# Kernel tuning notes

Measured on AMD Instinct MI355X. Metric: run time of the kernel, lower is better.

The kernel has to match this reference:

```python
import jax, jax.numpy as jnp
import numpy as np
import math

B, S, D, H = 8, 2048, 1024, 16
DH = D // H  # attention head size = 64

def setup_inputs() -> dict:
    key = jax.random.key(0)
    ks = jax.random.split(key, 10)
    s = 1.0 / math.sqrt(D)
    return {
        "hidden_states": jax.random.normal(ks[0], (B, S, D), dtype=jnp.float32),
        "attention_mask": jnp.zeros((B, 1, S), dtype=jnp.float32),
        "Wq": jax.random.normal(ks[1], (D, D), dtype=jnp.float32) * s,
        "bq": jnp.zeros((D,), dtype=jnp.float32),
        "Wqa": jax.random.normal(ks[2], (D, H), dtype=jnp.float32) * s,
        "bqa": jnp.zeros((H,), dtype=jnp.float32),
        "Wk": jax.random.normal(ks[3], (D, D), dtype=jnp.float32) * s,
        "bk": jnp.zeros((D,), dtype=jnp.float32),
        "Wt": jax.random.normal(ks[4], (D, D), dtype=jnp.float32) * s,
        "bt": jnp.zeros((D,), dtype=jnp.float32),
    }

def reference(hidden_states, attention_mask, Wq, bq, Wqa, bqa, Wk, bk, Wt, bt):
    scale = 1.0 / math.sqrt(DH)
    q = hidden_states @ Wq + bq                      # [B,S,D] mixed_query_layer
    k = hidden_states @ Wk + bk                      # [B,S,D] mixed_key_layer
    # query attention logits -> [B,H,S]
    q_score = jnp.swapaxes(q @ Wqa + bqa, 1, 2) * scale + attention_mask
    q_weight = jax.nn.softmax(q_score, axis=-1)      # [B,H,S]
    ql = jnp.swapaxes(q.reshape(B, S, H, DH), 1, 2)  # [B,H,S,DH]
    kl = jnp.swapaxes(k.reshape(B, S, H, DH), 1, 2)  # [B,H,S,DH]
    pooled_q = jnp.einsum('bhs,bhsd->bhd', q_weight, ql)          # [B,H,DH]
    qk_score = jnp.einsum('bhsd,bhd->bhs', kl, pooled_q) * scale + attention_mask
    qk_weight = jax.nn.softmax(qk_score, axis=-1)                 # [B,H,S]
    pooled_k = jnp.einsum('bhs,bhsd->bhd', qk_weight, kl)         # [B,H,DH]
    weighted = pooled_k[:, :, None, :] * ql                       # [B,H,S,DH]
    weighted = jnp.swapaxes(weighted, 1, 2).reshape(B, S, D)      # [B,S,D]
    out = weighted @ Wt + bt + q                                  # transform + residual to query
    return out
```

## Files before the change

### kernel.cpp

```cpp
#include <hip/hip_runtime.h>
#include <hip/hip_bf16.h>
#include <math.h>

#define BB 8
#define SS 2048
#define DD 1024
#define HH 16
#define DHH 64
#define NROWS (BB*SS)
#define QSLICE ((size_t)BB * HH * SS)

typedef unsigned short u16;
typedef __attribute__((ext_vector_type(8))) __bf16 bf16x8;
typedef __attribute__((ext_vector_type(4))) float f32x4;

__device__ __forceinline__ u16 f2bf(float f) {
    union { float f; unsigned u; } v; v.f = f;
    unsigned r = v.u + 0x7fffu + ((v.u >> 16) & 1u);
    return (u16)(r >> 16);
}
__device__ __forceinline__ float bf2f(u16 b) {
    union { unsigned u; float f; } v; v.u = ((unsigned)b) << 16;
    return v.f;
}

__device__ __forceinline__ void load_lds16(const void* g, void* l) {
    __builtin_amdgcn_global_load_lds(
        (const __attribute__((address_space(1))) unsigned int*)g,
        (__attribute__((address_space(3))) unsigned int*)l,
        16, 0, 0);
}

__global__ __launch_bounds__(256) void cast_bf16_kernel(const float* __restrict__ in,
                                                        u16* __restrict__ out, int n4) {
    int i = blockIdx.x * 256 + threadIdx.x;
    if (i >= n4) return;
    float4 v = ((const float4*)in)[i];
    ushort4 o;
    o.x = f2bf(v.x); o.y = f2bf(v.y); o.z = f2bf(v.z); o.w = f2bf(v.w);
    ((ushort4*)out)[i] = o;
}

__global__ __launch_bounds__(256) void transpose_cast_kernel(const float* __restrict__ W,
                                                             u16* __restrict__ WT) {
    __shared__ float tile[32][33];
    int m0 = blockIdx.x * 32, k0 = blockIdx.y * 32;
    int tx = threadIdx.x & 31, ty = threadIdx.x >> 5;
    #pragma unroll
    for (int i = 0; i < 4; i++) {
        int kk = ty + i * 8;
        tile[kk][tx] = W[(k0 + kk) * DD + m0 + tx];
    }
    __syncthreads();
    #pragma unroll
    for (int i = 0; i < 4; i++) {
        int mm = ty + i * 8;
        WT[(m0 + mm) * DD + k0 + tx] = f2bf(tile[tx][mm]);
    }
}

__global__ __launch_bounds__(256) void wqa_transpose_kernel(const float* __restrict__ Wqa,
                                                            u16* __restrict__ WqaT) {
    int i = blockIdx.x * 256 + threadIdx.x;
    int h = i >> 10, k = i & 1023;
    WqaT[i] = f2bf(Wqa[k * HH + h]);
}

template<int MODE>
__global__ __launch_bounds__(256)
void gemm_kernel(const u16* __restrict__ A, const u16* __restrict__ BT,
                 const float* __restrict__ bias, const u16* __restrict__ res,
                 float* __restrict__ Cf, u16* __restrict__ Cb) {
    __shared__ u16 sA[128 * 64];
    __shared__ u16 sB[128 * 64];
    const int row0 = blockIdx.x * 128;
    const int col0 = blockIdx.y * 128;
    const int t = threadIdx.x;
    const int w = t >> 6, lane = t & 63;
    const int wr = (w >> 1) * 64, wc = (w & 1) * 64;
    const int m16 = lane & 15, quad = lane >> 4;

    f32x4 acc[4][4];
    #pragma unroll
    for (int i = 0; i < 4; i++)
        #pragma unroll
        for (int j = 0; j < 4; j++)
            acc[i][j] = (f32x4){0.f, 0.f, 0.f, 0.f};

    const int srow = t >> 3;
    const int scol = ((t & 7) ^ (srow & 7)) * 8;
    const u16* Ag = A + (size_t)(row0 + srow) * DD + scol;
    const u16* Bg = BT + (size_t)(col0 + srow) * DD + scol;

    for (int k0 = 0; k0 < DD; k0 += 64) {
        __syncthreads();
        #pragma unroll
        for (int j = 0; j < 4; j++) {
            load_lds16(Ag + k0 + (size_t)j * 32 * DD, &sA[j * 2048 + t * 8]);
            load_lds16(Bg + k0 + (size_t)j * 32 * DD, &sB[j * 2048 + t * 8]);
        }
        __syncthreads();
        #pragma unroll
        for (int ks = 0; ks < 2; ks++) {
            const int cpos = ((ks * 4 + quad) ^ (m16 & 7)) * 8;
            bf16x8 af[4], bfr[4];
            #pragma unroll
            for (int i = 0; i < 4; i++) {
                af[i]  = *(const bf16x8*)&sA[(wr + i * 16 + m16) * 64 + cpos];
                bfr[i] = *(const bf16x8*)&sB[(wc + i * 16 + m16) * 64 + cpos];
            }
            #pragma unroll
            for (int mi = 0; mi < 4; mi++)
                #pragma unroll
                for (int ni = 0; ni < 4; ni++)
                    acc[mi][ni] = __builtin_amdgcn_mfma_f32_16x16x32_bf16(
                        af[mi], bfr[ni], acc[mi][ni], 0, 0, 0);
        }
    }

    #pragma unroll
    for (int mi = 0; mi < 4; mi++) {
        #pragma unroll
        for (int r = 0; r < 4; r++) {
            int row = row0 + wr + mi * 16 + quad * 4 + r;
            #pragma unroll
            for (int ni = 0; ni < 4; ni++) {
                int col = col0 + wc + ni * 16 + m16;
                float v = acc[mi][ni][r] + bias[col];
                size_t idx = (size_t)row * DD + col;
                if (MODE == 1) Cb[idx] = f2bf(v);
                else Cf[idx] = v + bf2f(res[idx]);
            }
        }
    }
}

__global__ __launch_bounds__(256)
void qscore_mfma_kernel(const u16* __restrict__ qbf, const u16* __restrict__ WqaT,
                        float* __restrict__ qraw) {
    int w = threadIdx.x >> 6, lane = threadIdx.x & 63;
    int row0 = blockIdx.x * 64 + w * 16;
    int kbase = blockIdx.y * 256;
    int m16 = lane & 15, quad = lane >> 4;
    f32x4 acc = (f32x4){0.f, 0.f, 0.f, 0.f};
    const u16* ap = qbf + (size_t)(row0 + m16) * DD + kbase + quad * 8;
    const u16* bp = WqaT + (size_t)m16 * DD + kbase + quad * 8;
    #pragma unroll
    for (int kk = 0; kk < 256; kk += 32) {
        bf16x8 a = *(const bf16x8*)(ap + kk);
        bf16x8 b = *(const bf16x8*)(bp + kk);
        acc = __builtin_amdgcn_mfma_f32_16x16x32_bf16(a, b, acc, 0, 0, 0);
    }
    #pragma unroll
    for (int r = 0; r < 4; r++) {
        int grow = row0 + quad * 4 + r;
        int b = grow >> 11, sidx = grow & 2047;
        qraw[((size_t)(blockIdx.y * BB + b) * HH + m16) * SS + sidx] = acc[r];
    }
}

template<bool EPI>
__global__ __launch_bounds__(256)
void softmax_kernel(float* __restrict__ score, const float* __restrict__ bqa,
                    const float* __restrict__ mask) {
    int bh = blockIdx.x;
    int b = bh >> 4, h = bh & 15;
    float* srow = score + ((size_t)bh << 11);
    __shared__ float rm[4], rs[4];
    int t = threadIdx.x;

    float v[8];
    float m = -1e30f;
    #pragma unroll
    for (int i = 0; i < 8; i++) {
        int off = t + i * 256;
        float x;
        if (EPI) {
            x = srow[off] + srow[off + QSLICE] + srow[off + 2 * QSLICE] + srow[off + 3 * QSLICE];
            x = (x + bqa[h]) * 0.125f + mask[b * SS + off];
        } else {
            x = srow[off];
        }
        v[i] = x; m = fmaxf(m, x);
    }
    #pragma unroll
    for (int off = 32; off; off >>= 1) m = fmaxf(m, __shfl_xor(m, off));
    if ((t & 63) == 0) rm[t >> 6] = m;
    __syncthreads();
    m = fmaxf(fmaxf(rm[0], rm[1]), fmaxf(rm[2], rm[3]));

    float sum = 0.f;
    #pragma unroll
    for (int i = 0; i < 8; i++) { v[i] = __expf(v[i] - m); sum += v[i]; }
    #pragma unroll
    for (int off = 32; off; off >>= 1) sum += __shfl_xor(sum, off);
    if ((t & 63) == 0) rs[t >> 6] = sum;
    __syncthreads();
    float inv = 1.0f / (rs[0] + rs[1] + rs[2] + rs[3]);
    #pragma unroll
    for (int i = 0; i < 8; i++) srow[t + i * 256] = v[i] * inv;
}

__global__ __launch_bounds__(256)
void pool_kernel(const float* __restrict__ w, const u16* __restrict__ X,
                 float* __restrict__ pooled) {
    int b = blockIdx.x;
    int s0 = blockIdx.y * 32;
    int t = threadIdx.x;
    int wid = t >> 6, lane = t & 63;
    int h = lane >> 2;
    __shared__ float sw[16 * 33];
    __shared__ float pr[4][64 * 17];
    {
        int hh = t >> 4, si = t & 15;
        const float* wr = w + ((size_t)(b * HH + hh) << 11) + s0;
        sw[hh * 33 + si] = wr[si];
        sw[hh * 33 + si + 16] = wr[si + 16];
    }
    __syncthreads();
    float acc[16];
    #pragma unroll
    for (int j = 0; j < 16; j++) acc[j] = 0.f;
    const u16* xbase = X + ((size_t)(b * SS + s0 + wid * 8) << 10) + lane * 16;
    #pragma unroll
    for (int rr = 0; rr < 8; rr++) {
        float ws = sw[h * 33 + wid * 8 + rr];
        const uint4* xp = (const uint4*)(xbase + (size_t)rr * DD);
        uint4 x0 = xp[0], x1 = xp[1];
        unsigned xw[8] = {x0.x, x0.y, x0.z, x0.w, x1.x, x1.y, x1.z, x1.w};
        #pragma unroll
        for (int i2 = 0; i2 < 8; i2++) {
            union { unsigned u; float f; } lo, hi;
            lo.u = xw[i2] << 16; hi.u = xw[i2] & 0xffff0000u;
            acc[2 * i2]     += ws * lo.f;
            acc[2 * i2 + 1] += ws * hi.f;
        }
    }
    #pragma unroll
    for (int j = 0; j < 16; j++) pr[wid][lane * 17 + j] = acc[j];
    __syncthreads();
    #pragma unroll
    for (int i = 0; i < 4; i++) {
        int idx = t + i * 256;
        int l2 = idx >> 4, j2 = idx & 15;
        float v = pr[0][l2 * 17 + j2] + pr[1][l2 * 17 + j2] +
                  pr[2][l2 * 17 + j2] + pr[3][l2 * 17 + j2];
        int od = (l2 >> 2) * 64 + (l2 & 3) * 16 + j2;
        atomicAdd(&pooled[b * DD + od], v);
    }
}

__global__ __launch_bounds__(256)
void qkscore_kernel(const u16* __restrict__ kbf, const float* __restrict__ pq,
                    const float* __restrict__ mask, float* __restrict__ qkscore) {
    int row = blockIdx.x * 4 + (threadIdx.x >> 6);
    int lane = threadIdx.x & 63;
    int b = row >> 11, s = row & 2047;
    int h = lane >> 2, dp = lane & 3;
    const u16* kp = kbf + (size_t)row * DD + h * 64 + dp * 16;
    const float* pqp = pq + (size_t)(b * HH + h) * 64 + dp * 16;
    const uint4* kp4 = (const uint4*)kp;
    uint4 ka = kp4[0], kb4 = kp4[1];
    unsigned kw[8] = {ka.x, ka.y, ka.z, ka.w, kb4.x, kb4.y, kb4.z, kb4.w};
    float acc = 0.f;
    #pragma unroll
    for (int i = 0; i < 8; i++) {
        union { unsigned u; float f; } lo, hi;
        lo.u = kw[i] << 16;
        hi.u = kw[i] & 0xffff0000u;
        acc += lo.f * pqp[2 * i] + hi.f * pqp[2 * i + 1];
    }
    acc += __shfl_xor(acc, 1);
    acc += __shfl_xor(acc, 2);
    if (dp == 0) qkscore[(size_t)(b * HH + h) * SS + s] = acc * 0.125f + mask[b * SS + s];
}

__global__ __launch_bounds__(256)
void weighted_kernel(const u16* __restrict__ qbf, const float* __restrict__ pk,
                     u16* __restrict__ wout) {
    int i = blockIdx.x * 256 + threadIdx.x;
    int row = i >> 8;
    int c0 = (i & 255) << 2;
    int b = row >> 11;
    int h = c0 >> 6, d = c0 & 63;
    ushort4 qv = ((const ushort4*)qbf)[i];
    const float4 pv = *(const float4*)(pk + (size_t)(b * HH + h) * 64 + d);
    ushort4 o;
    o.x = f2bf(bf2f(qv.x) * pv.x); o.y = f2bf(bf2f(qv.y) * pv.y);
    o.z = f2bf(bf2f(qv.z) * pv.z); o.w = f2bf(bf2f(qv.w) * pv.w);
    ((ushort4*)wout)[i] = o;
}

extern "C" void kernel_launch(void* const* d_in, const int* in_sizes, int n_in,
                              void* d_out, int out_size, void* d_ws, size_t ws_size,
                              hipStream_t stream) {
    const float* hs   = (const float*)d_in[0];
    const float* mask = (const float*)d_in[1];
    const float* Wq   = (const float*)d_in[2];
    const float* bq   = (const float*)d_in[3];
    const float* Wqa  = (const float*)d_in[4];
    const float* bqa  = (const float*)d_in[5];
    const float* Wk   = (const float*)d_in[6];
    const float* bk   = (const float*)d_in[7];
    const float* Wt   = (const float*)d_in[8];
    const float* bt   = (const float*)d_in[9];
    float* out = (float*)d_out;

    char* ws = (char*)d_ws;
    u16*   hs_bf = (u16*)ws;   ws += (size_t)NROWS * DD * 2;
    u16*   WqT   = (u16*)ws;   ws += (size_t)DD * DD * 2;
    u16*   WkT   = (u16*)ws;   ws += (size_t)DD * DD * 2;
    u16*   WtT   = (u16*)ws;   ws += (size_t)DD * DD * 2;
    u16*   WqaT  = (u16*)ws;   ws += (size_t)HH * DD * 2;
    u16*   q_bf  = (u16*)ws;   ws += (size_t)NROWS * DD * 2;
    u16*   k_bf  = (u16*)ws;   ws += (size_t)NROWS * DD * 2;
    float* qraw  = (float*)ws; ws += QSLICE * 4 * 4;
    float* qksc  = (float*)ws; ws += (size_t)BB * HH * SS * 4;
    float* pq    = (float*)ws; ws += (size_t)BB * HH * 64 * 4;
    float* pk    = (float*)ws; ws += (size_t)BB * HH * 64 * 4;
    u16*   wbf   = hs_bf;

    int n4 = NROWS * DD / 4;
    cast_bf16_kernel<<<n4 / 256, 256, 0, stream>>>(hs, hs_bf, n4);
    transpose_cast_kernel<<<dim3(32, 32), 256, 0, stream>>>(Wq, WqT);
    transpose_cast_kernel<<<dim3(32, 32), 256, 0, stream>>>(Wk, WkT);
    transpose_cast_kernel<<<dim3(32, 32), 256, 0, stream>>>(Wt, WtT);
    wqa_transpose_kernel<<<HH * DD / 256, 256, 0, stream>>>(Wqa, WqaT);

    hipMemsetAsync(pq, 0, (size_t)BB * HH * 64 * 4, stream);
    hipMemsetAsync(pk, 0, (size_t)BB * HH * 64 * 4, stream);

    gemm_kernel<1><<<dim3(NROWS / 128, DD / 128), 256, 0, stream>>>(hs_bf, WqT, bq, nullptr, nullptr, q_bf);
    gemm_kernel<1><<<dim3(NROWS / 128, DD / 128), 256, 0, stream>>>(hs_bf, WkT, bk, nullptr, nullptr, k_bf);

    qscore_mfma_kernel<<<dim3(NROWS / 64, 4), 256, 0, stream>>>(q_bf, WqaT, qraw);
    softmax_kernel<true><<<BB * HH, 256, 0, stream>>>(qraw, bqa, mask);
    pool_kernel<<<dim3(BB, SS / 32), 256, 0, stream>>>(qraw, q_bf, pq);
    qkscore_kernel<<<NROWS / 4, 256, 0, stream>>>(k_bf, pq, mask, qksc);
    softmax_kernel<false><<<BB * HH, 256, 0, stream>>>(qksc, nullptr, nullptr);
    pool_kernel<<<dim3(BB, SS / 32), 256, 0, stream>>>(qksc, k_bf, pk);
    weighted_kernel<<<n4 / 256, 256, 0, stream>>>(q_bf, pk, wbf);

    gemm_kernel<2><<<dim3(NROWS / 128, DD / 128), 256, 0, stream>>>(wbf, WtT, bt, q_bf, out, nullptr);
}
```

Baseline: 333.6 us.

## Use 256x256 double-buffered GEMM tiles with 512-thread blocks

Replaces the 128x128 single-buffered bf16 MFMA GEMM with a 256x256 tile kernel run by 8 waves. It double-buffers LDS, prefetching the next K-slice with async global-to-LDS loads while the current one is computed, and synchronises with explicit vmcnt waits and barriers. The goal is more operand reuse per LDS load and hiding global load latency behind MFMA work. In exchange each thread holds 128 accumulator floats, and the block needs 128KB of LDS. The launch bound asks for two blocks per CU, which tightens the register limit and risks spills.

```diff
diff --git a/kernel.cpp b/kernel.cpp
--- a/kernel.cpp
+++ b/kernel.cpp
@@ -30,6 +30,10 @@
         (__attribute__((address_space(3))) unsigned int*)l,
         16, 0, 0);
 }
+
+#define BAR() do { asm volatile("" ::: "memory"); \
+                   __builtin_amdgcn_s_barrier();  \
+                   asm volatile("" ::: "memory"); } while (0)
 
 __global__ __launch_bounds__(256) void cast_bf16_kernel(const float* __restrict__ in,
                                                         u16* __restrict__ out, int n4) {
@@ -67,22 +71,22 @@
 }
 
 template<int MODE>
-__global__ __launch_bounds__(256)
-void gemm_kernel(const u16* __restrict__ A, const u16* __restrict__ BT,
-                 const float* __restrict__ bias, const u16* __restrict__ res,
-                 float* __restrict__ Cf, u16* __restrict__ Cb) {
-    __shared__ u16 sA[128 * 64];
-    __shared__ u16 sB[128 * 64];
-    const int row0 = blockIdx.x * 128;
-    const int col0 = blockIdx.y * 128;
+__global__ __launch_bounds__(512, 2)
+void gemm256_kernel(const u16* __restrict__ A, const u16* __restrict__ BT,
+                    const float* __restrict__ bias, const u16* __restrict__ res,
+                    float* __restrict__ Cf, u16* __restrict__ Cb) {
+    __shared__ u16 sA[2][256 * 64];
+    __shared__ u16 sB[2][256 * 64];
+    const int row0 = blockIdx.x * 256;
+    const int col0 = blockIdx.y * 256;
     const int t = threadIdx.x;
     const int w = t >> 6, lane = t & 63;
-    const int wr = (w >> 1) * 64, wc = (w & 1) * 64;
+    const int wm = w >> 2, wn = w & 3;
     const int m16 = lane & 15, quad = lane >> 4;
 
-    f32x4 acc[4][4];
-    #pragma unroll
-    for (int i = 0; i < 4; i++)
+    f32x4 acc[8][4];
+    #pragma unroll
+    for (int i = 0; i < 8; i++)
         #pragma unroll
         for (int j = 0; j < 4; j++)
             acc[i][j] = (f32x4){0.f, 0.f, 0.f, 0.f};
@@ -92,40 +96,58 @@
     const u16* Ag = A + (size_t)(row0 + srow) * DD + scol;
     const u16* Bg = BT + (size_t)(col0 + srow) * DD + scol;
 
-    for (int k0 = 0; k0 < DD; k0 += 64) {
-        __syncthreads();
-        #pragma unroll
-        for (int j = 0; j < 4; j++) {
-            load_lds16(Ag + k0 + (size_t)j * 32 * DD, &sA[j * 2048 + t * 8]);
-            load_lds16(Bg + k0 + (size_t)j * 32 * DD, &sB[j * 2048 + t * 8]);
-        }
-        __syncthreads();
-        #pragma unroll
-        for (int ks = 0; ks < 2; ks++) {
+    auto STAGE = [&](int buf, int k0) {
+        #pragma unroll
+        for (int j = 0; j < 4; ++j) {
+            load_lds16(Ag + k0 + (size_t)j * 64 * DD, &sA[buf][j * 4096 + t * 8]);
+            load_lds16(Bg + k0 + (size_t)j * 64 * DD, &sB[buf][j * 4096 + t * 8]);
+        }
+    };
+
+    STAGE(0, 0);
+    STAGE(1, 64);
+    asm volatile("s_waitcnt vmcnt(8)" ::: "memory");
+    BAR();
+
+    for (int kt = 0; kt < 16; ++kt) {
+        const int cur = kt & 1;
+        const u16* sAc = sA[cur];
+        const u16* sBc = sB[cur];
+        #pragma unroll
+        for (int ks = 0; ks < 2; ++ks) {
             const int cpos = ((ks * 4 + quad) ^ (m16 & 7)) * 8;
-            bf16x8 af[4], bfr[4];
+            bf16x8 af[8], bfr[4];
             #pragma unroll
-            for (int i = 0; i < 4; i++) {
-                af[i]  = *(const bf16x8*)&sA[(wr + i * 16 + m16) * 64 + cpos];
-                bfr[i] = *(const bf16x8*)&sB[(wc + i * 16 + m16) * 64 + cpos];
-            }
+            for (int mi = 0; mi < 8; ++mi)
+                af[mi] = *(const bf16x8*)&sAc[(wm * 128 + mi * 16 + m16) * 64 + cpos];
             #pragma unroll
-            for (int mi = 0; mi < 4; mi++)
+            for (int ni = 0; ni < 4; ++ni)
+                bfr[ni] = *(const bf16x8*)&sBc[(wn * 64 + ni * 16 + m16) * 64 + cpos];
+            #pragma unroll
+            for (int mi = 0; mi < 8; ++mi)
                 #pragma unroll
-                for (int ni = 0; ni < 4; ni++)
+                for (int ni = 0; ni < 4; ++ni)
                     acc[mi][ni] = __builtin_amdgcn_mfma_f32_16x16x32_bf16(
                         af[mi], bfr[ni], acc[mi][ni], 0, 0, 0);
         }
-    }
-
-    #pragma unroll
-    for (int mi = 0; mi < 4; mi++) {
-        #pragma unroll
-        for (int r = 0; r < 4; r++) {
-            int row = row0 + wr + mi * 16 + quad * 4 + r;
+        BAR();
+        if (kt < 14) {
+            STAGE(cur, (kt + 2) * 64);
+            asm volatile("s_waitcnt vmcnt(8)" ::: "memory");
+        } else {
+            asm volatile("s_waitcnt vmcnt(0)" ::: "memory");
+        }
+        BAR();
+    }
+
+    #pragma unroll
+    for (int mi = 0; mi < 8; ++mi) {
+        #pragma unroll
+        for (int r = 0; r < 4; ++r) {
+            int row = row0 + wm * 128 + mi * 16 + quad * 4 + r;
             #pragma unroll
-            for (int ni = 0; ni < 4; ni++) {
-                int col = col0 + wc + ni * 16 + m16;
+            for (int ni = 0; ni < 4; ++ni) {
+                int col = col0 + wn * 64 + ni * 16 + m16;
                 float v = acc[mi][ni][r] + bias[col];
                 size_t idx = (size_t)row * DD + col;
                 if (MODE == 1) Cb[idx] = f2bf(v);
@@ -330,8 +352,8 @@
     hipMemsetAsync(pq, 0, (size_t)BB * HH * 64 * 4, stream);
     hipMemsetAsync(pk, 0, (size_t)BB * HH * 64 * 4, stream);
 
-    gemm_kernel<1><<<dim3(NROWS / 128, DD / 128), 256, 0, stream>>>(hs_bf, WqT, bq, nullptr, nullptr, q_bf);
-    gemm_kernel<1><<<dim3(NROWS / 128, DD / 128), 256, 0, stream>>>(hs_bf, WkT, bk, nullptr, nullptr, k_bf);
+    gemm256_kernel<1><<<dim3(NROWS / 256, DD / 256), 512, 0, stream>>>(hs_bf, WqT, bq, nullptr, nullptr, q_bf);
+    gemm256_kernel<1><<<dim3(NROWS / 256, DD / 256), 512, 0, stream>>>(hs_bf, WkT, bk, nullptr, nullptr, k_bf);
 
     qscore_mfma_kernel<<<dim3(NROWS / 64, 4), 256, 0, stream>>>(q_bf, WqaT, qraw);
     softmax_kernel<true><<<BB * HH, 256, 0, stream>>>(qraw, bqa, mask);
@@ -341,5 +363,5 @@
     pool_kernel<<<dim3(BB, SS / 32), 256, 0, stream>>>(qksc, k_bf, pk);
     weighted_kernel<<<n4 / 256, 256, 0, stream>>>(q_bf, pk, wbf);
 
-    gemm_kernel<2><<<dim3(NROWS / 128, DD / 128), 256, 0, stream>>>(wbf, WtT, bt, q_bf, out, nullptr);
-}
+    gemm256_kernel<2><<<dim3(NROWS / 256, DD / 256), 512, 0, stream>>>(wbf, WtT, bt, q_bf, out, nullptr);
+}
```

New measurement: 319.8 us. 1.04x faster.
